# Optimization experiments

Hardware: AMD Instinct MI355X
Metric: run time of the kernel (lower is better)

The kernel has to match this reference:

```python
import jax, jax.numpy as jnp
import numpy as np
import math

B, T, C, H, D = 4, 2048, 1024, 16, 64  # batch, seq, n_embd, n_head, head_dim


def setup_inputs() -> dict:
    key = jax.random.key(0)
    kx, kq, kk, kv, ko = jax.random.split(key, 5)
    x = jax.random.normal(kx, (B, T, C), dtype=jnp.float32)
    # standard RoPE tables, half head_dim
    d = D // 2
    inv_freq = 1.0 / (10000.0 ** (jnp.arange(d, dtype=jnp.float32) / d))
    freqs = jnp.outer(jnp.arange(T, dtype=jnp.float32), inv_freq)  # [T, d]
    cos = jnp.cos(freqs)[None, None]  # [1,1,T,d]
    sin = jnp.sin(freqs)[None, None]
    s = 0.02
    Wq = jax.random.normal(kq, (C, C), dtype=jnp.float32) * s  # stored [in,out]
    Wk = jax.random.normal(kk, (C, C), dtype=jnp.float32) * s
    Wv = jax.random.normal(kv, (C, C), dtype=jnp.float32) * s
    Wo = jax.random.normal(ko, (C, C), dtype=jnp.float32) * s
    return {"x": x, "cos": cos, "sin": sin, "Wq": Wq, "Wk": Wk, "Wv": Wv, "Wo": Wo}


def _rope(u, cos, sin):
    # u: [B,H,T,D]; rotate-half style RoPE matching apply_rotary_emb
    d = u.shape[-1] // 2
    u1, u2 = u[..., :d], u[..., d:]
    return jnp.concatenate([u1 * cos + u2 * sin, -u1 * sin + u2 * cos], axis=-1)


def _rms_norm(u):
    # parameter-free RMSNorm, eps = finfo eps (torch F.rms_norm default)
    eps = jnp.finfo(u.dtype).eps
    return u * jax.lax.rsqrt(jnp.mean(u * u, axis=-1, keepdims=True) + eps)


def reference(x, cos, sin, Wq, Wk, Wv, Wo):
    b, t, c = x.shape

    def split_heads(h):
        return h.reshape(b, t, H, D).transpose(0, 2, 1, 3)  # [B,H,T,D]

    q = split_heads(x @ Wq)
    k = split_heads(x @ Wk)
    v = split_heads(x @ Wv)
    q = _rms_norm(_rope(q, cos, sin))
    k = _rms_norm(_rope(k, cos, sin))
    scale = 1.0 / math.sqrt(D)
    scores = jnp.einsum('bhqd,bhkd->bhqk', q, k) * scale  # [B,H,T,T]
    causal = jnp.tril(jnp.ones((t, t), dtype=bool))
    scores = jnp.where(causal, scores, -jnp.inf)
    attn = jax.nn.softmax(scores, axis=-1)
    y = jnp.einsum('bhqk,bhkd->bhqd', attn, v)
    y = y.transpose(0, 2, 1, 3).reshape(b, t, c)
    return y @ Wo
```

## Files before the change

### kernel.cpp

```cpp
#include <hip/hip_runtime.h>


typedef __attribute__((ext_vector_type(8))) short short8;
typedef __attribute__((ext_vector_type(4))) short short4v;
typedef __attribute__((ext_vector_type(4))) float f32x4;

__device__ __forceinline__ unsigned short f2b(float f) {
  union { float f; unsigned int i; } x; x.f = f;
  return (unsigned short)((x.i + 0x7FFFu + ((x.i >> 16) & 1u)) >> 16);
}

__device__ __forceinline__ unsigned short b16(float f) {
  return __builtin_bit_cast(unsigned short, (__bf16)f);
}

__device__ __forceinline__ void glds16(const void* g, void* l) {
  __builtin_amdgcn_global_load_lds((const __attribute__((address_space(1))) unsigned int*)g,
                                   (__attribute__((address_space(3))) unsigned int*)l,
                                   16, 0, 0);
}

__device__ __forceinline__ f32x4 mfma16(short8 a, short8 b, f32x4 c) {
  return __builtin_amdgcn_mfma_f32_16x16x32_bf16(a, b, c, 0, 0, 0);
}

__global__ __launch_bounds__(256) void cast_x_kernel(const float* __restrict__ x,
                                                     unsigned short* __restrict__ xb) {
  const long i = ((long)blockIdx.x * 256 + threadIdx.x) * 8;
  const float4 a = *(const float4*)(x + i);
  const float4 b = *(const float4*)(x + i + 4);
  unsigned short o[8] = {f2b(a.x), f2b(a.y), f2b(a.z), f2b(a.w),
                         f2b(b.x), f2b(b.y), f2b(b.z), f2b(b.w)};
  *(short8*)(xb + i) = *(const short8*)o;
}

__global__ __launch_bounds__(256) void transpose_cast_w(
    const float* __restrict__ W0, const float* __restrict__ W1,
    const float* __restrict__ W2, const float* __restrict__ W3,
    unsigned short* __restrict__ Wt, unsigned short* __restrict__ Wot) {
  const int z = blockIdx.z;
  const float* __restrict__ W = (z == 0) ? W0 : (z == 1) ? W1 : (z == 2) ? W2 : W3;
  unsigned short* __restrict__ dst = (z < 3) ? (Wt + (size_t)z * 1024 * 1024) : Wot;
  __shared__ float tile[32][33];
  const int tx = threadIdx.x, ty = threadIdx.y;
  const int bx = blockIdx.x * 32, by = blockIdx.y * 32;
#pragma unroll
  for (int i = 0; i < 4; ++i)
    tile[ty + 8 * i][tx] = W[(size_t)(by + ty + 8 * i) * 1024 + bx + tx];
  __syncthreads();
#pragma unroll
  for (int i = 0; i < 4; ++i)
    dst[(size_t)(bx + ty + 8 * i) * 1024 + by + tx] = f2b(tile[tx][ty + 8 * i]);
}

__global__ __launch_bounds__(256) void gemm_qkv(
    const unsigned short* __restrict__ A, const unsigned short* __restrict__ Bt,
    unsigned short* __restrict__ Qr, unsigned short* __restrict__ Kr,
    unsigned short* __restrict__ Vr,
    const float* __restrict__ cosp, const float* __restrict__ sinp) {
  __shared__ unsigned short As[128 * 64];
  __shared__ unsigned short Bs[128 * 64];
  const int tid = threadIdx.x;
  const int wave = tid >> 6, lane = tid & 63;
  const int ln = lane & 15, grp = lane >> 4;
  const int wr = wave >> 1, wc = wave & 1;
  const int row0 = blockIdx.x * 128, col0 = blockIdx.y * 128;

  f32x4 acc[4][4];
  const f32x4 z4 = {0.f, 0.f, 0.f, 0.f};
#pragma unroll
  for (int m = 0; m < 4; ++m)
#pragma unroll
    for (int n = 0; n < 4; ++n) acc[m][n] = z4;

  const int sw = (ln & 7) << 4;

  for (int k0 = 0; k0 < 1024; k0 += 64) {
    __syncthreads();
#pragma unroll
    for (int it = 0; it < 4; ++it) {
      const int cl = it * 256 + tid;
      const int r = cl >> 3;
      const int sc = ((cl & 7) ^ (r & 7)) * 8;
      glds16(A + (long)(row0 + r) * 1024 + k0 + sc, (char*)As + it * 4096 + wave * 1024);
      glds16(Bt + (long)(col0 + r) * 1024 + k0 + sc, (char*)Bs + it * 4096 + wave * 1024);
    }
    __syncthreads();
#pragma unroll
    for (int ks = 0; ks < 2; ++ks) {
      short8 af[4], bfv[4];
#pragma unroll
      for (int m = 0; m < 4; ++m) {
        const int row = wr * 64 + m * 16 + ln;
        af[m] = *(const short8*)((const char*)As + row * 128 + ((grp * 16 + ks * 64) ^ sw));
      }
#pragma unroll
      for (int n = 0; n < 4; ++n) {
        const int row = wc * 64 + n * 16 + ln;
        bfv[n] = *(const short8*)((const char*)Bs + row * 128 + ((grp * 16 + ks * 64) ^ sw));
      }
#pragma unroll
      for (int m = 0; m < 4; ++m)
#pragma unroll
        for (int n = 0; n < 4; ++n)
          acc[m][n] = mfma16(af[m], bfv[n], acc[m][n]);
    }
  }

  const int colbase = col0 + wc * 64;
  const int z = colbase >> 10;
  const int h = (colbase & 1023) >> 6;
  unsigned short* __restrict__ dst = (z == 0) ? Qr : (z == 1) ? Kr : Vr;

  if (z < 2) {
    const float qs = (z == 0) ? 0.125f * 1.44269504f : 1.0f;
#pragma unroll
    for (int m = 0; m < 4; ++m) {
#pragma unroll
      for (int reg = 0; reg < 4; ++reg) {
        const int row = row0 + wr * 64 + m * 16 + grp * 4 + reg;
        const int t = row & 2047, b = row >> 11;
        const float u0 = acc[m][0][reg], u1 = acc[m][1][reg];
        const float u2 = acc[m][2][reg], u3 = acc[m][3][reg];
        const float c0 = cosp[t * 32 + ln],      s0 = sinp[t * 32 + ln];
        const float c1 = cosp[t * 32 + 16 + ln], s1 = sinp[t * 32 + 16 + ln];
        const float r0 =  u0 * c0 + u2 * s0;
        const float r1 =  u1 * c1 + u3 * s1;
        const float r2 = -u0 * s0 + u2 * c0;
        const float r3 = -u1 * s1 + u3 * c1;
        float ss = r0 * r0 + r1 * r1 + r2 * r2 + r3 * r3;
        ss += __shfl_xor(ss, 1); ss += __shfl_xor(ss, 2);
        ss += __shfl_xor(ss, 4); ss += __shfl_xor(ss, 8);
        const float inv = rsqrtf(ss * (1.0f / 64.0f) + 1.1920929e-07f) * qs;
        const long base = (((long)(b * 16 + h)) * 2048 + t) * 64;
        dst[base + ln]      = f2b(r0 * inv);
        dst[base + 16 + ln] = f2b(r1 * inv);
        dst[base + 32 + ln] = f2b(r2 * inv);
        dst[base + 48 + ln] = f2b(r3 * inv);
      }
    }
  } else {
#pragma unroll
    for (int m = 0; m < 4; ++m) {
#pragma unroll
      for (int reg = 0; reg < 4; ++reg) {
        const int row = row0 + wr * 64 + m * 16 + grp * 4 + reg;
        const int t = row & 2047, b = row >> 11;
        const long base = (((long)(b * 16 + h)) * 2048 + t) * 64;
#pragma unroll
        for (int n = 0; n < 4; ++n)
          dst[base + n * 16 + ln] = f2b(acc[m][n][reg]);
      }
    }
  }
}

__global__ __launch_bounds__(256) void attn_kernel(
    const unsigned short* __restrict__ Q, const unsigned short* __restrict__ K,
    const unsigned short* __restrict__ V, unsigned short* __restrict__ Y) {
  __shared__ unsigned short lds[2 * 8192];
  const int tid = threadIdx.x;
  const int wave = tid >> 6, lane = tid & 63;
  const int ln = lane & 15, grp = lane >> 4;

  const int linb = blockIdx.x;
  const int xcd = linb & 7, slot = linb >> 3;
  const int bh = xcd * 8 + (slot >> 4);
  const int pr = slot & 15;

  const long bhT = (long)bh * 2048;
  const int b = bh >> 4, h = bh & 15;
  auto* lds3 = (__attribute__((address_space(3))) unsigned short*)lds;

  const short o1 = (short)0x3f80;
  const short8 ones = {o1, o1, o1, o1, o1, o1, o1, o1};

  auto stage = [&](int j, int buf) {
    const long kvoff = bhT + (long)j * 64;
    char* Kb = (char*)lds + buf * 16384;
#pragma unroll
    for (int p = 0; p < 2; ++p) {
      const int cl = p * 256 + tid;
      const int krow = cl >> 3;
      const int kcb = ((cl & 7) * 16) ^ ((krow & 7) << 4);
      glds16(K + (kvoff + krow) * 64 + (kcb >> 1), Kb + p * 4096 + wave * 1024);
      const int dtv = cl >> 7, kvt = (cl >> 3) & 15, rr = (cl >> 1) & 3, hf = cl & 1;
      glds16(V + (kvoff + kvt * 4 + rr) * 64 + dtv * 16 + hf * 8,
             Kb + 8192 + p * 4096 + wave * 1024);
    }
  };

  const f32x4 z4 = {0.f, 0.f, 0.f, 0.f};

  for (int half = 0; half < 2; ++half) {
    const int bx = (half == 0) ? pr : 31 - pr;
    const int qw = bx * 64 + wave * 16;
    const int jmax = bx;

    short8 qf[2];
#pragma unroll
    for (int c = 0; c < 2; ++c)
      qf[c] = *(const short8*)(Q + (bhT + qw + ln) * 64 + c * 32 + grp * 8);

    f32x4 accO[4];
#pragma unroll
    for (int dt = 0; dt < 4; ++dt) accO[dt] = z4;
    f32x4 accL = z4;

    stage(0, 0);
    asm volatile("s_waitcnt vmcnt(0)" ::: "memory");
    __builtin_amdgcn_s_barrier();

    int cur = 0;
    for (int j = 0; j <= jmax; ++j, cur ^= 1) {
      if (j < jmax) {
        stage(j + 1, cur ^ 1);
        asm volatile("s_waitcnt vmcnt(4)" ::: "memory");
      } else {
        asm volatile("s_waitcnt vmcnt(0)" ::: "memory");
      }
      __builtin_amdgcn_s_barrier();

      const unsigned short* Kb = lds + cur * 8192;
      const bool maskp = (j == jmax);

      f32x4 sacc[4];
#pragma unroll
      for (int ct = 0; ct < 4; ++ct) sacc[ct] = z4;
      __builtin_amdgcn_s_setprio(1);
#pragma unroll
      for (int ct = 0; ct < 4; ++ct) {
        const int row = ct * 16 + ln;
        const int sw = (ln & 7) << 4;
        const char* rp = (const char*)Kb + row * 128;
        const short8 kf0 = *(const short8*)(rp + ((grp * 16) ^ sw));
        const short8 kf1 = *(const short8*)(rp + ((grp * 16 + 64) ^ sw));
        sacc[ct] = mfma16(kf0, qf[0], sacc[ct]);
        sacc[ct] = mfma16(kf1, qf[1], sacc[ct]);
      }
      __builtin_amdgcn_s_setprio(0);

      short8 pf[2];
      {
        if (maskp) {
          const int q = qw + ln;
#pragma unroll
          for (int ct = 0; ct < 4; ++ct)
#pragma unroll
            for (int r = 0; r < 4; ++r) {
              const int kv = j * 64 + ct * 16 + grp * 4 + r;
              if (kv > q) sacc[ct][r] = -INFINITY;
            }
        }
#pragma unroll
        for (int ct = 0; ct < 4; ++ct)
#pragma unroll
          for (int r = 0; r < 4; ++r)
            pf[ct >> 1][(ct & 1) * 4 + r] = (short)b16(exp2f(sacc[ct][r]));
      }

      const unsigned vb = (unsigned)(size_t)&lds3[cur * 8192 + 4096] + (unsigned)lane * 8;
      short4v t[4][4];
#pragma unroll
      for (int dt = 0; dt < 4; ++dt) {
        const unsigned va = vb + dt * 2048;
        asm volatile("ds_read_b64_tr_b16 %0, %4 offset:0\n\t"
                     "ds_read_b64_tr_b16 %1, %4 offset:512\n\t"
                     "ds_read_b64_tr_b16 %2, %4 offset:1024\n\t"
                     "ds_read_b64_tr_b16 %3, %4 offset:1536"
                     : "=&v"(t[dt][0]), "=&v"(t[dt][1]), "=&v"(t[dt][2]), "=&v"(t[dt][3])
                     : "v"(va));
      }
      asm volatile("s_waitcnt lgkmcnt(0)" ::: "memory");
      __builtin_amdgcn_sched_barrier(0);
      __builtin_amdgcn_s_setprio(1);
#pragma unroll
      for (int dt = 0; dt < 4; ++dt) {
        const short8 vf0 = __builtin_shufflevector(t[dt][0], t[dt][1], 0, 1, 2, 3, 4, 5, 6, 7);
        const short8 vf1 = __builtin_shufflevector(t[dt][2], t[dt][3], 0, 1, 2, 3, 4, 5, 6, 7);
        accO[dt] = mfma16(vf0, pf[0], accO[dt]);
        accO[dt] = mfma16(vf1, pf[1], accO[dt]);
      }
      accL = mfma16(ones, pf[0], accL);
      accL = mfma16(ones, pf[1], accL);
      __builtin_amdgcn_s_setprio(0);
      __builtin_amdgcn_s_barrier();
    }

    {
      const float inv = 1.0f / accL[0];
      const int t_ = qw + ln;
      const long base = (((long)(b * 2048 + t_)) * 16 + h) * 64;
#pragma unroll
      for (int dt = 0; dt < 4; ++dt) {
        unsigned short o[4];
#pragma unroll
        for (int r = 0; r < 4; ++r) o[r] = b16(accO[dt][r] * inv);
        *(short4v*)(Y + base + dt * 16 + grp * 4) = *(const short4v*)o;
      }
    }
  }
}

__global__ __launch_bounds__(256) void gemm_out(
    const unsigned short* __restrict__ A, const unsigned short* __restrict__ Bt,
    float* __restrict__ C) {
  __shared__ unsigned short As[128 * 64];
  __shared__ unsigned short Bs[128 * 64];
  const int tid = threadIdx.x;
  const int wave = tid >> 6, lane = tid & 63;
  const int ln = lane & 15, grp = lane >> 4;
  const int wr = wave >> 1, wc = wave & 1;
  const int row0 = blockIdx.x * 128, col0 = blockIdx.y * 128;

  f32x4 acc[4][4];
  const f32x4 z4 = {0.f, 0.f, 0.f, 0.f};
#pragma unroll
  for (int m = 0; m < 4; ++m)
#pragma unroll
    for (int n = 0; n < 4; ++n) acc[m][n] = z4;

  const int sw = (ln & 7) << 4;

  for (int k0 = 0; k0 < 1024; k0 += 64) {
    __syncthreads();
#pragma unroll
    for (int it = 0; it < 4; ++it) {
      const int cl = it * 256 + tid;
      const int r = cl >> 3;
      const int sc = ((cl & 7) ^ (r & 7)) * 8;
      glds16(A + (long)(row0 + r) * 1024 + k0 + sc, (char*)As + it * 4096 + wave * 1024);
      glds16(Bt + (long)(col0 + r) * 1024 + k0 + sc, (char*)Bs + it * 4096 + wave * 1024);
    }
    __syncthreads();
#pragma unroll
    for (int ks = 0; ks < 2; ++ks) {
      short8 af[4], bfv[4];
#pragma unroll
      for (int m = 0; m < 4; ++m) {
        const int row = wr * 64 + m * 16 + ln;
        af[m] = *(const short8*)((const char*)As + row * 128 + ((grp * 16 + ks * 64) ^ sw));
      }
#pragma unroll
      for (int n = 0; n < 4; ++n) {
        const int row = wc * 64 + n * 16 + ln;
        bfv[n] = *(const short8*)((const char*)Bs + row * 128 + ((grp * 16 + ks * 64) ^ sw));
      }
#pragma unroll
      for (int m = 0; m < 4; ++m)
#pragma unroll
        for (int n = 0; n < 4; ++n)
          acc[m][n] = mfma16(af[m], bfv[n], acc[m][n]);
    }
  }

#pragma unroll
  for (int m = 0; m < 4; ++m)
#pragma unroll
    for (int reg = 0; reg < 4; ++reg) {
      const int row = row0 + wr * 64 + m * 16 + grp * 4 + reg;
#pragma unroll
      for (int n = 0; n < 4; ++n)
        C[(long)row * 1024 + col0 + wc * 64 + n * 16 + ln] = acc[m][n][reg];
    }
}

extern "C" void kernel_launch(void* const* d_in, const int* in_sizes, int n_in,
                              void* d_out, int out_size, void* d_ws, size_t ws_size,
                              hipStream_t stream) {
  (void)in_sizes; (void)n_in; (void)out_size; (void)ws_size;
  const float* x    = (const float*)d_in[0];
  const float* cosp = (const float*)d_in[1];
  const float* sinp = (const float*)d_in[2];
  const float* Wq   = (const float*)d_in[3];
  const float* Wk   = (const float*)d_in[4];
  const float* Wv   = (const float*)d_in[5];
  const float* Wo   = (const float*)d_in[6];
  float* out = (float*)d_out;

  unsigned short* xb  = (unsigned short*)d_ws;
  unsigned short* Wt  = xb  + (size_t)8192 * 1024;
  unsigned short* Wot = Wt  + (size_t)3 * 1024 * 1024;
  unsigned short* Qr  = Wot + (size_t)1024 * 1024;
  unsigned short* Kr  = Qr  + (size_t)8192 * 1024;
  unsigned short* Vr  = Kr  + (size_t)8192 * 1024;
  unsigned short* Yb  = xb;

  cast_x_kernel<<<4096, 256, 0, stream>>>(x, xb);
  transpose_cast_w<<<dim3(32, 32, 4), dim3(32, 8), 0, stream>>>(Wq, Wk, Wv, Wo, Wt, Wot);
  gemm_qkv<<<dim3(64, 24), 256, 0, stream>>>(xb, Wt, Qr, Kr, Vr, cosp, sinp);
  attn_kernel<<<1024, 256, 0, stream>>>(Qr, Kr, Vr, Yb);
  gemm_out<<<dim3(64, 8), 256, 0, stream>>>(Yb, Wot, out);
}
```

Measured before the change: 179.7 us.

## Process paired query tiles in one KV sweep to share K/V loads

The attention kernel used to handle its two paired query blocks (pr and 31-pr) in two separate passes over the KV tiles, loading K/V for the short block again. Now both query blocks are processed together in one loop over the longer block's KV range, and the short block's MFMAs are predicated on j <= bxA. This removes the duplicate K/V staging and LDS traffic for the shared prefix, and gives more independent MFMA work per barrier. The cost is doubled accumulator registers, which may lower occupancy, plus divergent-free but branchy predication.

Result: slower. 186.3 us (+3.7%).

```diff
diff --git a/kernel.cpp b/kernel.cpp
--- a/kernel.cpp
+++ b/kernel.cpp
@@ -192,112 +192,147 @@
 
   const f32x4 z4 = {0.f, 0.f, 0.f, 0.f};
 
-  for (int half = 0; half < 2; ++half) {
-    const int bx = (half == 0) ? pr : 31 - pr;
-    const int qw = bx * 64 + wave * 16;
-    const int jmax = bx;
-
-    short8 qf[2];
-#pragma unroll
-    for (int c = 0; c < 2; ++c)
-      qf[c] = *(const short8*)(Q + (bhT + qw + ln) * 64 + c * 32 + grp * 8);
-
-    f32x4 accO[4];
-#pragma unroll
-    for (int dt = 0; dt < 4; ++dt) accO[dt] = z4;
-    f32x4 accL = z4;
-
-    stage(0, 0);
-    asm volatile("s_waitcnt vmcnt(0)" ::: "memory");
+  const int bxA = pr, bxB = 31 - pr;
+  const int qwA = bxA * 64 + wave * 16;
+  const int qwB = bxB * 64 + wave * 16;
+  const int jmax = bxB;
+
+  short8 qfA[2], qfB[2];
+#pragma unroll
+  for (int c = 0; c < 2; ++c) {
+    qfA[c] = *(const short8*)(Q + (bhT + qwA + ln) * 64 + c * 32 + grp * 8);
+    qfB[c] = *(const short8*)(Q + (bhT + qwB + ln) * 64 + c * 32 + grp * 8);
+  }
+
+  f32x4 accOA[4], accOB[4];
+#pragma unroll
+  for (int dt = 0; dt < 4; ++dt) { accOA[dt] = z4; accOB[dt] = z4; }
+  f32x4 accLA = z4, accLB = z4;
+
+  stage(0, 0);
+  asm volatile("s_waitcnt vmcnt(0)" ::: "memory");
+  __builtin_amdgcn_s_barrier();
+
+  int cur = 0;
+  for (int j = 0; j <= jmax; ++j, cur ^= 1) {
+    if (j < jmax) {
+      stage(j + 1, cur ^ 1);
+      asm volatile("s_waitcnt vmcnt(4)" ::: "memory");
+    } else {
+      asm volatile("s_waitcnt vmcnt(0)" ::: "memory");
+    }
     __builtin_amdgcn_s_barrier();
 
-    int cur = 0;
-    for (int j = 0; j <= jmax; ++j, cur ^= 1) {
-      if (j < jmax) {
-        stage(j + 1, cur ^ 1);
-        asm volatile("s_waitcnt vmcnt(4)" ::: "memory");
-      } else {
-        asm volatile("s_waitcnt vmcnt(0)" ::: "memory");
-      }
-      __builtin_amdgcn_s_barrier();
-
-      const unsigned short* Kb = lds + cur * 8192;
-      const bool maskp = (j == jmax);
-
-      f32x4 sacc[4];
-#pragma unroll
-      for (int ct = 0; ct < 4; ++ct) sacc[ct] = z4;
-      __builtin_amdgcn_s_setprio(1);
-#pragma unroll
-      for (int ct = 0; ct < 4; ++ct) {
-        const int row = ct * 16 + ln;
-        const int sw = (ln & 7) << 4;
-        const char* rp = (const char*)Kb + row * 128;
-        const short8 kf0 = *(const short8*)(rp + ((grp * 16) ^ sw));
-        const short8 kf1 = *(const short8*)(rp + ((grp * 16 + 64) ^ sw));
-        sacc[ct] = mfma16(kf0, qf[0], sacc[ct]);
-        sacc[ct] = mfma16(kf1, qf[1], sacc[ct]);
-      }
-      __builtin_amdgcn_s_setprio(0);
-
-      short8 pf[2];
-      {
-        if (maskp) {
-          const int q = qw + ln;
-#pragma unroll
-          for (int ct = 0; ct < 4; ++ct)
-#pragma unroll
-            for (int r = 0; r < 4; ++r) {
-              const int kv = j * 64 + ct * 16 + grp * 4 + r;
-              if (kv > q) sacc[ct][r] = -INFINITY;
-            }
-        }
+    const unsigned short* Kb = lds + cur * 8192;
+    const bool actA = (j <= bxA);
+    const bool maskA = (j == bxA);
+    const bool maskB = (j == jmax);
+
+    f32x4 sa[4], sb[4];
+#pragma unroll
+    for (int ct = 0; ct < 4; ++ct) { sa[ct] = z4; sb[ct] = z4; }
+    __builtin_amdgcn_s_setprio(1);
+#pragma unroll
+    for (int ct = 0; ct < 4; ++ct) {
+      const int row = ct * 16 + ln;
+      const int sw = (ln & 7) << 4;
+      const char* rp = (const char*)Kb + row * 128;
+      const short8 kf0 = *(const short8*)(rp + ((grp * 16) ^ sw));
+      const short8 kf1 = *(const short8*)(rp + ((grp * 16 + 64) ^ sw));
+      sb[ct] = mfma16(kf0, qfB[0], sb[ct]);
+      sb[ct] = mfma16(kf1, qfB[1], sb[ct]);
+      if (actA) {
+        sa[ct] = mfma16(kf0, qfA[0], sa[ct]);
+        sa[ct] = mfma16(kf1, qfA[1], sa[ct]);
+      }
+    }
+    __builtin_amdgcn_s_setprio(0);
+
+    short8 pfA[2], pfB[2];
+    if (actA) {
+      if (maskA) {
+        const int q = qwA + ln;
 #pragma unroll
         for (int ct = 0; ct < 4; ++ct)
 #pragma unroll
-          for (int r = 0; r < 4; ++r)
-            pf[ct >> 1][(ct & 1) * 4 + r] = (short)b16(exp2f(sacc[ct][r]));
-      }
-
-      const unsigned vb = (unsigned)(size_t)&lds3[cur * 8192 + 4096] + (unsigned)lane * 8;
-      short4v t[4][4];
-#pragma unroll
-      for (int dt = 0; dt < 4; ++dt) {
-        const unsigned va = vb + dt * 2048;
-        asm volatile("ds_read_b64_tr_b16 %0, %4 offset:0\n\t"
-                     "ds_read_b64_tr_b16 %1, %4 offset:512\n\t"
-                     "ds_read_b64_tr_b16 %2, %4 offset:1024\n\t"
-                     "ds_read_b64_tr_b16 %3, %4 offset:1536"
-                     : "=&v"(t[dt][0]), "=&v"(t[dt][1]), "=&v"(t[dt][2]), "=&v"(t[dt][3])
-                     : "v"(va));
-      }
-      asm volatile("s_waitcnt lgkmcnt(0)" ::: "memory");
-      __builtin_amdgcn_sched_barrier(0);
-      __builtin_amdgcn_s_setprio(1);
-#pragma unroll
-      for (int dt = 0; dt < 4; ++dt) {
-        const short8 vf0 = __builtin_shufflevector(t[dt][0], t[dt][1], 0, 1, 2, 3, 4, 5, 6, 7);
-        const short8 vf1 = __builtin_shufflevector(t[dt][2], t[dt][3], 0, 1, 2, 3, 4, 5, 6, 7);
-        accO[dt] = mfma16(vf0, pf[0], accO[dt]);
-        accO[dt] = mfma16(vf1, pf[1], accO[dt]);
-      }
-      accL = mfma16(ones, pf[0], accL);
-      accL = mfma16(ones, pf[1], accL);
-      __builtin_amdgcn_s_setprio(0);
-      __builtin_amdgcn_s_barrier();
-    }
-
+          for (int r = 0; r < 4; ++r) {
+            const int kv = j * 64 + ct * 16 + grp * 4 + r;
+            if (kv > q) sa[ct][r] = -INFINITY;
+          }
+      }
+#pragma unroll
+      for (int ct = 0; ct < 4; ++ct)
+#pragma unroll
+        for (int r = 0; r < 4; ++r)
+          pfA[ct >> 1][(ct & 1) * 4 + r] = (short)b16(exp2f(sa[ct][r]));
+    }
     {
-      const float inv = 1.0f / accL[0];
-      const int t_ = qw + ln;
-      const long base = (((long)(b * 2048 + t_)) * 16 + h) * 64;
-#pragma unroll
-      for (int dt = 0; dt < 4; ++dt) {
-        unsigned short o[4];
-#pragma unroll
-        for (int r = 0; r < 4; ++r) o[r] = b16(accO[dt][r] * inv);
-        *(short4v*)(Y + base + dt * 16 + grp * 4) = *(const short4v*)o;
-      }
+      if (maskB) {
+        const int q = qwB + ln;
+#pragma unroll
+        for (int ct = 0; ct < 4; ++ct)
+#pragma unroll
+          for (int r = 0; r < 4; ++r) {
+            const int kv = j * 64 + ct * 16 + grp * 4 + r;
+            if (kv > q) sb[ct][r] = -INFINITY;
+          }
+      }
+#pragma unroll
+      for (int ct = 0; ct < 4; ++ct)
+#pragma unroll
+        for (int r = 0; r < 4; ++r)
+          pfB[ct >> 1][(ct & 1) * 4 + r] = (short)b16(exp2f(sb[ct][r]));
+    }
+
+    const unsigned vb = (unsigned)(size_t)&lds3[cur * 8192 + 4096] + (unsigned)lane * 8;
+    short4v t[4][4];
+#pragma unroll
+    for (int dt = 0; dt < 4; ++dt) {
+      const unsigned va = vb + dt * 2048;
+      asm volatile("ds_read_b64_tr_b16 %0, %4 offset:0\n\t"
+                   "ds_read_b64_tr_b16 %1, %4 offset:512\n\t"
+                   "ds_read_b64_tr_b16 %2, %4 offset:1024\n\t"
+                   "ds_read_b64_tr_b16 %3, %4 offset:1536"
+                   : "=&v"(t[dt][0]), "=&v"(t[dt][1]), "=&v"(t[dt][2]), "=&v"(t[dt][3])
+                   : "v"(va));
+    }
+    asm volatile("s_waitcnt lgkmcnt(0)" ::: "memory");
+    __builtin_amdgcn_sched_barrier(0);
+    __builtin_amdgcn_s_setprio(1);
+#pragma unroll
+    for (int dt = 0; dt < 4; ++dt) {
+      const short8 vf0 = __builtin_shufflevector(t[dt][0], t[dt][1], 0, 1, 2, 3, 4, 5, 6, 7);
+      const short8 vf1 = __builtin_shufflevector(t[dt][2], t[dt][3], 0, 1, 2, 3, 4, 5, 6, 7);
+      accOB[dt] = mfma16(vf0, pfB[0], accOB[dt]);
+      accOB[dt] = mfma16(vf1, pfB[1], accOB[dt]);
+      if (actA) {
+        accOA[dt] = mfma16(vf0, pfA[0], accOA[dt]);
+        accOA[dt] = mfma16(vf1, pfA[1], accOA[dt]);
+      }
+    }
+    accLB = mfma16(ones, pfB[0], accLB);
+    accLB = mfma16(ones, pfB[1], accLB);
+    if (actA) {
+      accLA = mfma16(ones, pfA[0], accLA);
+      accLA = mfma16(ones, pfA[1], accLA);
+    }
+    __builtin_amdgcn_s_setprio(0);
+    __builtin_amdgcn_s_barrier();
+  }
+
+#pragma unroll
+  for (int s = 0; s < 2; ++s) {
+    const int qw = s ? qwB : qwA;
+    const f32x4* accO = s ? accOB : accOA;
+    const float inv = 1.0f / (s ? accLB[0] : accLA[0]);
+    const int t_ = qw + ln;
+    const long base = (((long)(b * 2048 + t_)) * 16 + h) * 64;
+#pragma unroll
+    for (int dt = 0; dt < 4; ++dt) {
+      unsigned short o[4];
+#pragma unroll
+      for (int r = 0; r < 4; ++r) o[r] = b16(accO[dt][r] * inv);
+      *(short4v*)(Y + base + dt * 16 + grp * 4) = *(const short4v*)o;
     }
   }
 }
```

## Pipeline QKV and output GEMM loads with 4-slot LDS ring buffer

Applied to the files above, without the earlier changes.

Replaces the single-buffered K=64 tile loop in both projection GEMMs with a 4-slot ring of K=32 tiles, prefetching three stages ahead via direct global-to-LDS loads and using explicit vmcnt waits plus one barrier per step. The aim is to overlap global memory latency with MFMA work instead of stalling at two syncthreads per tile. It also drops the XOR swizzle, so the 64-byte rows may now cause LDS bank conflicts, and it raises MFMA priority with s_setprio. Correctness depends on the hand-counted vmcnt values matching the number of outstanding loads.

Result: slower. 194.0 us (+8.0%).

```diff
diff --git a/kernel.cpp b/kernel.cpp
--- a/kernel.cpp
+++ b/kernel.cpp
@@ -58,8 +58,8 @@
     unsigned short* __restrict__ Qr, unsigned short* __restrict__ Kr,
     unsigned short* __restrict__ Vr,
     const float* __restrict__ cosp, const float* __restrict__ sinp) {
-  __shared__ unsigned short As[128 * 64];
-  __shared__ unsigned short Bs[128 * 64];
+  __shared__ unsigned short As[4 * 128 * 32];
+  __shared__ unsigned short Bs[4 * 128 * 32];
   const int tid = threadIdx.x;
   const int wave = tid >> 6, lane = tid & 63;
   const int ln = lane & 15, grp = lane >> 4;
@@ -73,38 +73,45 @@
 #pragma unroll
     for (int n = 0; n < 4; ++n) acc[m][n] = z4;
 
-  const int sw = (ln & 7) << 4;
-
-  for (int k0 = 0; k0 < 1024; k0 += 64) {
-    __syncthreads();
-#pragma unroll
-    for (int it = 0; it < 4; ++it) {
-      const int cl = it * 256 + tid;
-      const int r = cl >> 3;
-      const int sc = ((cl & 7) ^ (r & 7)) * 8;
-      glds16(A + (long)(row0 + r) * 1024 + k0 + sc, (char*)As + it * 4096 + wave * 1024);
-      glds16(Bt + (long)(col0 + r) * 1024 + k0 + sc, (char*)Bs + it * 4096 + wave * 1024);
-    }
-    __syncthreads();
-#pragma unroll
-    for (int ks = 0; ks < 2; ++ks) {
-      short8 af[4], bfv[4];
-#pragma unroll
-      for (int m = 0; m < 4; ++m) {
-        const int row = wr * 64 + m * 16 + ln;
-        af[m] = *(const short8*)((const char*)As + row * 128 + ((grp * 16 + ks * 64) ^ sw));
-      }
-#pragma unroll
-      for (int n = 0; n < 4; ++n) {
-        const int row = wc * 64 + n * 16 + ln;
-        bfv[n] = *(const short8*)((const char*)Bs + row * 128 + ((grp * 16 + ks * 64) ^ sw));
-      }
-#pragma unroll
-      for (int m = 0; m < 4; ++m)
-#pragma unroll
-        for (int n = 0; n < 4; ++n)
-          acc[m][n] = mfma16(af[m], bfv[n], acc[m][n]);
-    }
+  auto stage = [&](int t) {
+    const int slot = t & 3;
+    char* Adst = (char*)As + slot * 8192;
+    char* Bdst = (char*)Bs + slot * 8192;
+    const int kbase = t * 32;
+#pragma unroll
+    for (int p = 0; p < 2; ++p) {
+      const int cl = p * 256 + tid;
+      const int r = cl >> 2;
+      const int cc = (cl & 3) * 8;
+      glds16(A + (long)(row0 + r) * 1024 + kbase + cc, Adst + p * 4096 + wave * 1024);
+      glds16(Bt + (long)(col0 + r) * 1024 + kbase + cc, Bdst + p * 4096 + wave * 1024);
+    }
+  };
+
+  stage(0); stage(1); stage(2);
+  for (int t = 0; t < 32; ++t) {
+    if (t <= 29)      asm volatile("s_waitcnt vmcnt(8)" ::: "memory");
+    else if (t == 30) asm volatile("s_waitcnt vmcnt(4)" ::: "memory");
+    else              asm volatile("s_waitcnt vmcnt(0)" ::: "memory");
+    __builtin_amdgcn_s_barrier();
+    if (t + 3 < 32) stage(t + 3);
+
+    const unsigned short* Asl = As + (t & 3) * 4096;
+    const unsigned short* Bsl = Bs + (t & 3) * 4096;
+    short8 af[4], bfv[4];
+#pragma unroll
+    for (int m = 0; m < 4; ++m)
+      af[m] = *(const short8*)&Asl[(wr * 64 + m * 16 + ln) * 32 + grp * 8];
+#pragma unroll
+    for (int n = 0; n < 4; ++n)
+      bfv[n] = *(const short8*)&Bsl[(wc * 64 + n * 16 + ln) * 32 + grp * 8];
+    __builtin_amdgcn_s_setprio(1);
+#pragma unroll
+    for (int m = 0; m < 4; ++m)
+#pragma unroll
+      for (int n = 0; n < 4; ++n)
+        acc[m][n] = mfma16(af[m], bfv[n], acc[m][n]);
+    __builtin_amdgcn_s_setprio(0);
   }
 
   const int colbase = col0 + wc * 64;
@@ -305,8 +312,8 @@
 __global__ __launch_bounds__(256) void gemm_out(
     const unsigned short* __restrict__ A, const unsigned short* __restrict__ Bt,
     float* __restrict__ C) {
-  __shared__ unsigned short As[128 * 64];
-  __shared__ unsigned short Bs[128 * 64];
+  __shared__ unsigned short As[4 * 128 * 32];
+  __shared__ unsigned short Bs[4 * 128 * 32];
   const int tid = threadIdx.x;
   const int wave = tid >> 6, lane = tid & 63;
   const int ln = lane & 15, grp = lane >> 4;
@@ -320,38 +327,45 @@
 #pragma unroll
     for (int n = 0; n < 4; ++n) acc[m][n] = z4;
 
-  const int sw = (ln & 7) << 4;
-
-  for (int k0 = 0; k0 < 1024; k0 += 64) {
-    __syncthreads();
-#pragma unroll
-    for (int it = 0; it < 4; ++it) {
-      const int cl = it * 256 + tid;
-      const int r = cl >> 3;
-      const int sc = ((cl & 7) ^ (r & 7)) * 8;
-      glds16(A + (long)(row0 + r) * 1024 + k0 + sc, (char*)As + it * 4096 + wave * 1024);
-      glds16(Bt + (long)(col0 + r) * 1024 + k0 + sc, (char*)Bs + it * 4096 + wave * 1024);
-    }
-    __syncthreads();
-#pragma unroll
-    for (int ks = 0; ks < 2; ++ks) {
-      short8 af[4], bfv[4];
-#pragma unroll
-      for (int m = 0; m < 4; ++m) {
-        const int row = wr * 64 + m * 16 + ln;
-        af[m] = *(const short8*)((const char*)As + row * 128 + ((grp * 16 + ks * 64) ^ sw));
-      }
-#pragma unroll
-      for (int n = 0; n < 4; ++n) {
-        const int row = wc * 64 + n * 16 + ln;
-        bfv[n] = *(const short8*)((const char*)Bs + row * 128 + ((grp * 16 + ks * 64) ^ sw));
-      }
-#pragma unroll
-      for (int m = 0; m < 4; ++m)
-#pragma unroll
-        for (int n = 0; n < 4; ++n)
-          acc[m][n] = mfma16(af[m], bfv[n], acc[m][n]);
-    }
+  auto stage = [&](int t) {
+    const int slot = t & 3;
+    char* Adst = (char*)As + slot * 8192;
+    char* Bdst = (char*)Bs + slot * 8192;
+    const int kbase = t * 32;
+#pragma unroll
+    for (int p = 0; p < 2; ++p) {
+      const int cl = p * 256 + tid;
+      const int r = cl >> 2;
+      const int cc = (cl & 3) * 8;
+      glds16(A + (long)(row0 + r) * 1024 + kbase + cc, Adst + p * 4096 + wave * 1024);
+      glds16(Bt + (long)(col0 + r) * 1024 + kbase + cc, Bdst + p * 4096 + wave * 1024);
+    }
+  };
+
+  stage(0); stage(1); stage(2);
+  for (int t = 0; t < 32; ++t) {
+    if (t <= 29)      asm volatile("s_waitcnt vmcnt(8)" ::: "memory");
+    else if (t == 30) asm volatile("s_waitcnt vmcnt(4)" ::: "memory");
+    else              asm volatile("s_waitcnt vmcnt(0)" ::: "memory");
+    __builtin_amdgcn_s_barrier();
+    if (t + 3 < 32) stage(t + 3);
+
+    const unsigned short* Asl = As + (t & 3) * 4096;
+    const unsigned short* Bsl = Bs + (t & 3) * 4096;
+    short8 af[4], bfv[4];
+#pragma unroll
+    for (int m = 0; m < 4; ++m)
+      af[m] = *(const short8*)&Asl[(wr * 64 + m * 16 + ln) * 32 + grp * 8];
+#pragma unroll
+    for (int n = 0; n < 4; ++n)
+      bfv[n] = *(const short8*)&Bsl[(wc * 64 + n * 16 + ln) * 32 + grp * 8];
+    __builtin_amdgcn_s_setprio(1);
+#pragma unroll
+    for (int m = 0; m < 4; ++m)
+#pragma unroll
+      for (int n = 0; n < 4; ++n)
+        acc[m][n] = mfma16(af[m], bfv[n], acc[m][n]);
+    __builtin_amdgcn_s_setprio(0);
   }
 
 #pragma unroll
```

## Rework QKV GEMM into 256x256 tiles with double-buffered async LDS pipeline

Applied to the files above, without the earlier changes.

The QKV projection GEMM now uses 512-thread blocks computing 256x256 output tiles (8 waves, each 128x64), up from 256-thread 128x128 tiles. Global-to-LDS loads are double-buffered and split into four quarter stages, interleaved with four MFMA phases and guarded by explicit vmcnt waits and barriers. MFMA bursts run at raised wave priority. The aim is to overlap memory loads with matrix math and improve operand reuse, at the cost of 128KB LDS per block, more accumulator registers, and a grid of only 384 blocks, which may underfill the CUs.

Measured after the change: 189.3 us. 5.3% more time.

```diff
diff --git a/kernel.cpp b/kernel.cpp
--- a/kernel.cpp
+++ b/kernel.cpp
@@ -53,58 +53,117 @@
     dst[(size_t)(bx + ty + 8 * i) * 1024 + by + tx] = f2b(tile[tx][ty + 8 * i]);
 }
 
-__global__ __launch_bounds__(256) void gemm_qkv(
+__global__ __launch_bounds__(512, 2) void gemm_qkv(
     const unsigned short* __restrict__ A, const unsigned short* __restrict__ Bt,
     unsigned short* __restrict__ Qr, unsigned short* __restrict__ Kr,
     unsigned short* __restrict__ Vr,
     const float* __restrict__ cosp, const float* __restrict__ sinp) {
-  __shared__ unsigned short As[128 * 64];
-  __shared__ unsigned short Bs[128 * 64];
+  __shared__ unsigned short As[2][2][128 * 64];
+  __shared__ unsigned short Bs[2][2][128 * 64];
   const int tid = threadIdx.x;
   const int wave = tid >> 6, lane = tid & 63;
   const int ln = lane & 15, grp = lane >> 4;
-  const int wr = wave >> 1, wc = wave & 1;
-  const int row0 = blockIdx.x * 128, col0 = blockIdx.y * 128;
-
-  f32x4 acc[4][4];
+  const int wr = wave >> 2, wc = wave & 3;
+  const int row0 = blockIdx.x * 256, col0 = blockIdx.y * 256;
+  const int sw = (ln & 7) << 4;
+
+  f32x4 acc[8][4];
   const f32x4 z4 = {0.f, 0.f, 0.f, 0.f};
 #pragma unroll
-  for (int m = 0; m < 4; ++m)
+  for (int m = 0; m < 8; ++m)
 #pragma unroll
     for (int n = 0; n < 4; ++n) acc[m][n] = z4;
 
-  const int sw = (ln & 7) << 4;
-
-  for (int k0 = 0; k0 < 1024; k0 += 64) {
-    __syncthreads();
-#pragma unroll
-    for (int it = 0; it < 4; ++it) {
-      const int cl = it * 256 + tid;
+  auto stageA = [&](int kt, int half) {
+    unsigned short* dst = As[kt & 1][half];
+#pragma unroll
+    for (int p = 0; p < 2; ++p) {
+      const int cl = p * 512 + tid;
       const int r = cl >> 3;
       const int sc = ((cl & 7) ^ (r & 7)) * 8;
-      glds16(A + (long)(row0 + r) * 1024 + k0 + sc, (char*)As + it * 4096 + wave * 1024);
-      glds16(Bt + (long)(col0 + r) * 1024 + k0 + sc, (char*)Bs + it * 4096 + wave * 1024);
-    }
-    __syncthreads();
-#pragma unroll
-    for (int ks = 0; ks < 2; ++ks) {
-      short8 af[4], bfv[4];
-#pragma unroll
-      for (int m = 0; m < 4; ++m) {
-        const int row = wr * 64 + m * 16 + ln;
-        af[m] = *(const short8*)((const char*)As + row * 128 + ((grp * 16 + ks * 64) ^ sw));
-      }
-#pragma unroll
-      for (int n = 0; n < 4; ++n) {
-        const int row = wc * 64 + n * 16 + ln;
-        bfv[n] = *(const short8*)((const char*)Bs + row * 128 + ((grp * 16 + ks * 64) ^ sw));
-      }
-#pragma unroll
-      for (int m = 0; m < 4; ++m)
-#pragma unroll
-        for (int n = 0; n < 4; ++n)
-          acc[m][n] = mfma16(af[m], bfv[n], acc[m][n]);
-    }
+      glds16(A + (long)(row0 + half * 128 + r) * 1024 + kt * 64 + sc,
+             (char*)dst + p * 8192 + wave * 1024);
+    }
+  };
+  auto stageB = [&](int kt, int half) {
+    unsigned short* dst = Bs[kt & 1][half];
+#pragma unroll
+    for (int p = 0; p < 2; ++p) {
+      const int cl = p * 512 + tid;
+      const int r = cl >> 3;
+      const int sc = ((cl & 7) ^ (r & 7)) * 8;
+      glds16(Bt + (long)(col0 + half * 128 + r) * 1024 + kt * 64 + sc,
+             (char*)dst + p * 8192 + wave * 1024);
+    }
+  };
+
+  auto phase = [&](int buf, int q) {
+    const int mh = q >> 1, nh = q & 1;
+    const unsigned short* Ah = As[buf][wr];
+    const unsigned short* Bh = Bs[buf][wc >> 1];
+    short8 af[4][2], bf[2][2];
+#pragma unroll
+    for (int i = 0; i < 4; ++i) {
+      const int row = (mh * 4 + i) * 16 + ln;
+      const char* rp = (const char*)Ah + row * 128;
+      af[i][0] = *(const short8*)(rp + ((grp * 16) ^ sw));
+      af[i][1] = *(const short8*)(rp + ((grp * 16 + 64) ^ sw));
+    }
+#pragma unroll
+    for (int j = 0; j < 2; ++j) {
+      const int row = (wc & 1) * 64 + (nh * 2 + j) * 16 + ln;
+      const char* rp = (const char*)Bh + row * 128;
+      bf[j][0] = *(const short8*)(rp + ((grp * 16) ^ sw));
+      bf[j][1] = *(const short8*)(rp + ((grp * 16 + 64) ^ sw));
+    }
+    __builtin_amdgcn_s_setprio(1);
+#pragma unroll
+    for (int i = 0; i < 4; ++i)
+#pragma unroll
+      for (int j = 0; j < 2; ++j) {
+        const int m = mh * 4 + i, n = nh * 2 + j;
+        acc[m][n] = mfma16(af[i][0], bf[j][0], acc[m][n]);
+        acc[m][n] = mfma16(af[i][1], bf[j][1], acc[m][n]);
+      }
+    __builtin_amdgcn_s_setprio(0);
+  };
+
+  stageA(0, 0); stageA(0, 1); stageB(0, 0); stageB(0, 1);
+  asm volatile("s_waitcnt vmcnt(0)" ::: "memory");
+  __builtin_amdgcn_s_barrier();
+
+  for (int it = 0; it < 8; ++it) {
+    const int kt = 2 * it;
+#pragma unroll
+    for (int q = 0; q < 4; ++q) {
+      if (q == 0) {
+        stageA(kt + 1, 0);
+        asm volatile("s_waitcnt vmcnt(2)" ::: "memory");
+      } else if (q == 1) stageA(kt + 1, 1);
+      else if (q == 2)  stageB(kt + 1, 0);
+      else              stageB(kt + 1, 1);
+      __builtin_amdgcn_s_barrier();
+      phase(0, q);
+    }
+    __builtin_amdgcn_s_barrier();
+#pragma unroll
+    for (int q = 0; q < 4; ++q) {
+      if (q == 0) {
+        if (it < 7) {
+          stageA(kt + 2, 0);
+          asm volatile("s_waitcnt vmcnt(2)" ::: "memory");
+        } else {
+          asm volatile("s_waitcnt vmcnt(0)" ::: "memory");
+        }
+      } else if (it < 7) {
+        if (q == 1)      stageA(kt + 2, 1);
+        else if (q == 2) stageB(kt + 2, 0);
+        else             stageB(kt + 2, 1);
+      }
+      __builtin_amdgcn_s_barrier();
+      phase(1, q);
+    }
+    __builtin_amdgcn_s_barrier();
   }
 
   const int colbase = col0 + wc * 64;
@@ -115,10 +174,10 @@
   if (z < 2) {
     const float qs = (z == 0) ? 0.125f * 1.44269504f : 1.0f;
 #pragma unroll
-    for (int m = 0; m < 4; ++m) {
+    for (int m = 0; m < 8; ++m) {
 #pragma unroll
       for (int reg = 0; reg < 4; ++reg) {
-        const int row = row0 + wr * 64 + m * 16 + grp * 4 + reg;
+        const int row = row0 + wr * 128 + m * 16 + grp * 4 + reg;
         const int t = row & 2047, b = row >> 11;
         const float u0 = acc[m][0][reg], u1 = acc[m][1][reg];
         const float u2 = acc[m][2][reg], u3 = acc[m][3][reg];
@@ -141,10 +200,10 @@
     }
   } else {
 #pragma unroll
-    for (int m = 0; m < 4; ++m) {
+    for (int m = 0; m < 8; ++m) {
 #pragma unroll
       for (int reg = 0; reg < 4; ++reg) {
-        const int row = row0 + wr * 64 + m * 16 + grp * 4 + reg;
+        const int row = row0 + wr * 128 + m * 16 + grp * 4 + reg;
         const int t = row & 2047, b = row >> 11;
         const long base = (((long)(b * 16 + h)) * 2048 + t) * 64;
 #pragma unroll
@@ -388,7 +447,7 @@
 
   cast_x_kernel<<<4096, 256, 0, stream>>>(x, xb);
   transpose_cast_w<<<dim3(32, 32, 4), dim3(32, 8), 0, stream>>>(Wq, Wk, Wv, Wo, Wt, Wot);
-  gemm_qkv<<<dim3(64, 24), 256, 0, stream>>>(xb, Wt, Qr, Kr, Vr, cosp, sinp);
+  gemm_qkv<<<dim3(32, 12), 512, 0, stream>>>(xb, Wt, Qr, Kr, Vr, cosp, sinp);
   attn_kernel<<<1024, 256, 0, stream>>>(Qr, Kr, Vr, Yb);
   gemm_out<<<dim3(64, 8), 256, 0, stream>>>(Yb, Wot, out);
 }
```
